# Kernel optimization log

Hardware: AMD Instinct MI355X
Metric: run time of the kernel (lower is better)

Reference implementation:

```python
import jax, jax.numpy as jnp
import numpy as np

# dims
B, N, M, R = 2, 16384, 512, 8      # batch, points, modes (slices), register tokens
D = 384                             # q_dim == kv_dim
H, DH = 8, 48                       # heads, dim_heads
P = 3                               # phys_dim
NF = DH // (2 * P)                  # rope freqs per physical axis (8)
FH = 1024                           # gated FFN hidden
L = 2                               # num_interleaved_layers
MINLF, MAXLF = -5.0, 3.0
EPS_LN = 1e-5
EPS_NORM = 1e-8


def _ln(x, g, b):
    m = jnp.mean(x, -1, keepdims=True)
    v = jnp.var(x, -1, keepdims=True)
    return (x - m) * jax.lax.rsqrt(v + EPS_LN) * g + b


def _rope_cs(coords):
    # coords: (B, S, P) -> cos/sin of shape (B, S, DH//2)
    freqs = jnp.exp(jnp.linspace(MINLF, MAXLF, NF))
    ang = (coords[..., :, None] * freqs).reshape(coords.shape[:-1] + (P * NF,))
    return jnp.cos(ang), jnp.sin(ang)


def _apply_rope(t, c, s):
    # t: (B, S, H, DH); c,s: (B, S, DH//2)
    tp = t.reshape(t.shape[:-1] + (DH // 2, 2))
    t0, t1 = tp[..., 0], tp[..., 1]
    c = c[:, :, None, :]
    s = s[:, :, None, :]
    r = jnp.stack([t0 * c - t1 * s, t0 * s + t1 * c], axis=-1)
    return r.reshape(t.shape)


def _mha(qin, kin, vin, xq, xk, wq, bq, wk, bk, wv, bv, wo, bo):
    Bq, Sq, _ = qin.shape
    Sk = kin.shape[1]
    q = (qin @ wq + bq).reshape(Bq, Sq, H, DH)
    k = (kin @ wk + bk).reshape(Bq, Sk, H, DH)
    v = (vin @ wv + bv).reshape(Bq, Sk, H, DH)
    cq, sq = _rope_cs(xq)
    ck, sk = _rope_cs(xk)
    q = _apply_rope(q, cq, sq)
    k = _apply_rope(k, ck, sk)
    scores = jnp.einsum('bqhd,bkhd->bhqk', q, k) / np.sqrt(DH).astype(np.float32)
    a = jax.nn.softmax(scores, axis=-1)
    o = jnp.einsum('bhqk,bkhd->bqhd', a, v).reshape(Bq, Sq, H * DH)
    return o @ wo + bo


def _subgen(feat, w, b):
    # Transolver slice generator: softmax over modes per point; mass == 1.
    tf = jax.nn.softmax(feat @ w + b, axis=-1)          # (B, S, M) trial_func
    tt = jnp.swapaxes(tf, 1, 2)                          # (B, M, S) trial_in_t
    inv = 1.0 / (jnp.sum(tf, axis=1) + EPS_NORM)         # (B, M) inv_trial_norm
    return tf, tt, inv[..., None]


def setup_inputs() -> dict:
    key = jax.random.key(0)
    ks = iter(jax.random.split(key, 64))
    nrm = lambda shape: jax.random.normal(next(ks), shape, dtype=jnp.float32)
    w = lambda shape: nrm(shape) * 0.02
    inp = {}
    inp['qx'] = nrm((B, N, D))
    inp['kvx'] = nrm((B, N, D))
    inp['x'] = jax.random.uniform(next(ks), (B, N, P), dtype=jnp.float32)
    inp['reg_tok_qx'] = nrm((B, R, D))
    inp['reg_tok_x'] = jax.random.uniform(next(ks), (B, R, P), dtype=jnp.float32)
    inp['subq_w'] = w((D, M)); inp['subq_b'] = jnp.zeros((M,))
    inp['subkv_w'] = w((D, M)); inp['subkv_b'] = jnp.zeros((M,))
    inp['nq_g'] = jnp.ones((D,)); inp['nq_b'] = jnp.zeros((D,))
    inp['nkv_g'] = jnp.ones((D,)); inp['nkv_b'] = jnp.zeros((D,))
    inp['a0_wq'] = w((D, H * DH)); inp['a0_bq'] = jnp.zeros((H * DH,))
    inp['a0_wk'] = w((D, H * DH)); inp['a0_bk'] = jnp.zeros((H * DH,))
    inp['a0_wv'] = w((D, H * DH)); inp['a0_bv'] = jnp.zeros((H * DH,))
    inp['a0_wo'] = w((H * DH, D)); inp['a0_bo'] = jnp.zeros((D,))
    inp['out_g'] = jnp.ones((D,)); inp['out_b'] = jnp.zeros((D,))
    inp['L_wq'] = w((L, D, H * DH)); inp['L_bq'] = jnp.zeros((L, H * DH))
    inp['L_wk'] = w((L, D, H * DH)); inp['L_bk'] = jnp.zeros((L, H * DH))
    inp['L_wv'] = w((L, D, H * DH)); inp['L_bv'] = jnp.zeros((L, H * DH))
    inp['L_wo'] = w((L, H * DH, D)); inp['L_bo'] = jnp.zeros((L, D))
    inp['L_ang'] = jnp.ones((L, D)); inp['L_anb'] = jnp.zeros((L, D))
    inp['L_fng'] = jnp.ones((L, D)); inp['L_fnb'] = jnp.zeros((L, D))
    inp['L_wg'] = w((L, D, FH)); inp['L_bg'] = jnp.zeros((L, FH))
    inp['L_wu'] = w((L, D, FH)); inp['L_bu'] = jnp.zeros((L, FH))
    inp['L_wd'] = w((L, FH, D)); inp['L_bd'] = jnp.zeros((L, D))
    return inp


def reference(qx, kvx, x, reg_tok_qx, reg_tok_x,
              subq_w, subq_b, subkv_w, subkv_b,
              nq_g, nq_b, nkv_g, nkv_b,
              a0_wq, a0_bq, a0_wk, a0_bk, a0_wv, a0_bv, a0_wo, a0_bo,
              out_g, out_b,
              L_wq, L_bq, L_wk, L_bk, L_wv, L_bv, L_wo, L_bo,
              L_ang, L_anb, L_fng, L_fnb,
              L_wg, L_bg, L_wu, L_bu, L_wd, L_bd):
    tfq, ttq, invq = _subgen(qx, subq_w, subq_b)
    _, ttkv, invkv = _subgen(kvx, subkv_w, subkv_b)
    qx_proj = jnp.matmul(ttq, qx) * invq          # (B, M, D)
    kvx_proj = jnp.matmul(ttkv, kvx) * invkv      # (B, M, D)
    xq_proj = jnp.matmul(ttq, x) * invq           # (B, M, P)
    xk_proj = jnp.matmul(ttkv, x) * invkv         # (B, M, P)
    q_full = jnp.concatenate([qx_proj, reg_tok_qx], axis=1)   # (B, M+R, D)
    xq_full = jnp.concatenate([xq_proj, reg_tok_x], axis=1)   # (B, M+R, P)
    q = _ln(q_full, nq_g, nq_b)
    kv = _ln(kvx_proj, nkv_g, nkv_b)
    y = _mha(q, kv, kv, xq_full, xk_proj,
             a0_wq, a0_bq, a0_wk, a0_bk, a0_wv, a0_bv, a0_wo, a0_bo) + q_full
    for i in range(L):
        h = _ln(y, L_fng[i], L_fnb[i])
        h = (jax.nn.silu(h @ L_wg[i] + L_bg[i]) * (h @ L_wu[i] + L_bu[i])) @ L_wd[i] + L_bd[i]
        y = h + y
        qn = _ln(y, L_ang[i], L_anb[i])
        y = _mha(qn, kv, kv, xq_full, xk_proj,
                 L_wq[i], L_bq[i], L_wk[i], L_bk[i], L_wv[i], L_bv[i], L_wo[i], L_bo[i]) + y
    y = _ln(y, out_g, out_b)
    y_proj = y[:, :M, :]
    reg_token = y[:, M:, :]
    y_recon = jnp.matmul(tfq, y_proj)             # (B, N, D)
    return (y_recon, reg_token)
```

## Files before the change

kernel.cpp:

```cpp
#include <hip/hip_runtime.h>


typedef __attribute__((ext_vector_type(8))) short short8;
typedef __attribute__((ext_vector_type(4))) float floatx4;

__device__ __forceinline__ float b2f(short s) {
    unsigned u = ((unsigned)(unsigned short)s) << 16;
    return __builtin_bit_cast(float, u);
}
__device__ __forceinline__ short f2b(float f) {
    unsigned u = __builtin_bit_cast(unsigned, f);
    unsigned r = (u + 0x7fffu + ((u >> 16) & 1u)) >> 16;
    return (short)r;
}

__device__ __forceinline__ void gload_lds16(const short* g, short* l) {
    __builtin_amdgcn_global_load_lds(
        (const __attribute__((address_space(1))) void*)(g),
        (__attribute__((address_space(3))) void*)(l), 16, 0, 0);
}

__global__ __launch_bounds__(256) void cvt_bf16(const float* __restrict__ src,
                                                short* __restrict__ dst, long n)
{
    long i = ((long)blockIdx.x * 256 + threadIdx.x) * 4;
    if (i + 4 <= n) {
        float4 v = *(const float4*)(src + i);
        short o[4] = {f2b(v.x), f2b(v.y), f2b(v.z), f2b(v.w)};
        *(short4*)(dst + i) = *(short4*)o;
    } else {
        for (long j = i; j < n; j++) dst[j] = f2b(src[j]);
    }
}

template <int EPI, bool SPLITK>
__global__ __launch_bounds__(256) void gemm_nt(
    const short* __restrict__ A, int lda, long sAb, long sAh,
    const short* __restrict__ Bm, int ldb, long sBb, long sBh,
    void* Cp, int ldc, long sCb, long sCh,
    const float* __restrict__ bias, int biasRow,
    const float* aux, int ldaux,
    int Mrows, int Ncols, int Kdim, int nb, int KC)
{
    int z = blockIdx.z;
    int b = z % nb;
    int rest = z / nb;
    long aoff = (long)b * sAb, boff = (long)b * sBb;
    long coff = (long)b * sCb + (long)rest * sCh;
    int k_begin = 0, kEnd = Kdim;
    if (SPLITK) {
        k_begin = rest * KC;
        int ke = k_begin + KC;
        kEnd = ke < Kdim ? ke : Kdim;
    } else {
        aoff += (long)rest * sAh;
        boff += (long)rest * sBh;
    }
    const short* Ap = A + aoff;
    const short* Bp = Bm + boff;

    int row0 = blockIdx.x * 128, col0 = blockIdx.y * 128;
    __shared__ __align__(16) short As[128 * 32];
    __shared__ __align__(16) short Bs[128 * 32];
    int tid = threadIdx.x, lane = tid & 63, wv = tid >> 6;
    int wr = (wv >> 1) * 64, wc = (wv & 1) * 64;
    int lr = lane & 15, lq = lane >> 4;

    const bool fullMN = (row0 + 128 <= Mrows) && (col0 + 128 <= Ncols);

    const int frow = (wv << 5) + (lane >> 2);
    const int fk = (lane & 3) << 3;
    const short* gA0 = Ap + (long)(row0 + frow) * lda + fk;
    const short* gA1 = gA0 + 16 * (long)lda;
    const short* gB0 = Bp + (long)(col0 + frow) * ldb + fk;
    const short* gB1 = gB0 + 16 * (long)ldb;
    short* lA0 = As + (wv << 10);
    short* lA1 = lA0 + 512;
    short* lB0 = Bs + (wv << 10);
    short* lB1 = lB0 + 512;

    floatx4 acc[4][4];
#pragma unroll
    for (int i = 0; i < 4; i++)
#pragma unroll
        for (int j = 0; j < 4; j++)
#pragma unroll
            for (int e = 0; e < 4; e++) acc[i][j][e] = 0.f;

    for (int k0 = k_begin; k0 < kEnd; k0 += 32) {
        __syncthreads();
        if (fullMN && (k0 + 32 <= kEnd)) {
            gload_lds16(gA0 + k0, lA0);
            gload_lds16(gA1 + k0, lA1);
            gload_lds16(gB0 + k0, lB0);
            gload_lds16(gB1 + k0, lB1);
        } else {
#pragma unroll
            for (int io = 0; io < 2; io++) {
                int sid = tid * 2 + io;
                int r = sid >> 2, sg = sid & 3;
                int gk = k0 + sg * 8;
                short8 va, vb;
#pragma unroll
                for (int j = 0; j < 8; j++) { va[j] = 0; vb[j] = 0; }
                int gra = row0 + r, grb = col0 + r;
                if (gra < Mrows) {
                    const short* p = Ap + (long)gra * lda + gk;
                    if (gk + 8 <= kEnd) va = *(const short8*)p;
                    else { for (int j = 0; j < 8; j++) if (gk + j < kEnd) va[j] = p[j]; }
                }
                if (grb < Ncols) {
                    const short* p = Bp + (long)grb * ldb + gk;
                    if (gk + 8 <= kEnd) vb = *(const short8*)p;
                    else { for (int j = 0; j < 8; j++) if (gk + j < kEnd) vb[j] = p[j]; }
                }
                *(short8*)&As[r * 32 + sg * 8] = va;
                *(short8*)&Bs[r * 32 + sg * 8] = vb;
            }
        }
        __syncthreads();
        short8 af[4], bfv[4];
#pragma unroll
        for (int mt = 0; mt < 4; mt++)
            af[mt] = *(const short8*)&As[(wr + mt * 16 + lr) * 32 + lq * 8];
#pragma unroll
        for (int nt = 0; nt < 4; nt++)
            bfv[nt] = *(const short8*)&Bs[(wc + nt * 16 + lr) * 32 + lq * 8];
#pragma unroll
        for (int mt = 0; mt < 4; mt++)
#pragma unroll
            for (int nt = 0; nt < 4; nt++)
                acc[mt][nt] = __builtin_amdgcn_mfma_f32_16x16x32_bf16(
                    af[mt], bfv[nt], acc[mt][nt], 0, 0, 0);
    }

    if (fullMN) {
#pragma unroll
        for (int mt = 0; mt < 4; mt++) {
#pragma unroll
            for (int nt = 0; nt < 4; nt++) {
                int gcol = col0 + wc + nt * 16 + lr;
#pragma unroll
                for (int r = 0; r < 4; r++) {
                    int grow = row0 + wr + mt * 16 + lq * 4 + r;
                    float v = acc[mt][nt][r];
                    if (bias) v += bias[biasRow ? grow : gcol];
                    long idx = coff + (long)grow * ldc + gcol;
                    if (EPI == 0) {
                        ((float*)Cp)[idx] = v;
                    } else if (EPI == 1) {
                        ((short*)Cp)[idx] = f2b(v);
                    } else if (EPI == 2) {
                        float g = aux[(long)grow * ldaux + gcol];
                        float sg = g / (1.f + __expf(-g));
                        ((short*)Cp)[idx] = f2b(sg * v);
                    } else {
                        float rr = aux[(long)grow * ldaux + gcol];
                        ((float*)Cp)[idx] = v + rr;
                    }
                }
            }
        }
    } else {
#pragma unroll
        for (int mt = 0; mt < 4; mt++) {
#pragma unroll
            for (int nt = 0; nt < 4; nt++) {
                int gcol = col0 + wc + nt * 16 + lr;
#pragma unroll
                for (int r = 0; r < 4; r++) {
                    int grow = row0 + wr + mt * 16 + lq * 4 + r;
                    if (grow < Mrows && gcol < Ncols) {
                        float v = acc[mt][nt][r];
                        if (bias) v += bias[biasRow ? grow : gcol];
                        long idx = coff + (long)grow * ldc + gcol;
                        if (EPI == 0) {
                            ((float*)Cp)[idx] = v;
                        } else if (EPI == 1) {
                            ((short*)Cp)[idx] = f2b(v);
                        } else if (EPI == 2) {
                            float g = aux[(long)grow * ldaux + gcol];
                            float sg = g / (1.f + __expf(-g));
                            ((short*)Cp)[idx] = f2b(sg * v);
                        } else {
                            float rr = aux[(long)grow * ldaux + gcol];
                            ((float*)Cp)[idx] = v + rr;
                        }
                    }
                }
            }
        }
    }
}

__global__ __launch_bounds__(256) void softmax_rows(
    const short* __restrict__ src, short* __restrict__ dstN,
    short* __restrict__ dstT, int rowsPerBatch)
{
    int n0 = blockIdx.x * 32;
    __shared__ __align__(16) short tile[32 * 512];
    int tid = threadIdx.x;
    const short8* gsrc = (const short8*)(src + (long)n0 * 512);
    short8* t8 = (short8*)tile;
#pragma unroll
    for (int i = 0; i < 8; i++) t8[tid + i * 256] = gsrc[tid + i * 256];
    __syncthreads();
    int wv = tid >> 6, lane = tid & 63;
#pragma unroll
    for (int rr = 0; rr < 8; rr++) {
        int r = wv * 8 + rr;
        short8 s = *(const short8*)&tile[r * 512 + lane * 8];
        float v[8];
        float mx = -1e30f;
#pragma unroll
        for (int j = 0; j < 8; j++) { v[j] = b2f(s[j]); mx = fmaxf(mx, v[j]); }
#pragma unroll
        for (int o = 32; o; o >>= 1) mx = fmaxf(mx, __shfl_xor(mx, o, 64));
        float sum = 0.f;
#pragma unroll
        for (int j = 0; j < 8; j++) { v[j] = __expf(v[j] - mx); sum += v[j]; }
#pragma unroll
        for (int o = 32; o; o >>= 1) sum += __shfl_xor(sum, o, 64);
        float inv = 1.0f / sum;
        short8 o8;
#pragma unroll
        for (int j = 0; j < 8; j++) o8[j] = f2b(v[j] * inv);
        *(short8*)&tile[r * 512 + lane * 8] = o8;
        if (dstN) *(short8*)(dstN + (long)(n0 + r) * 512 + lane * 8) = o8;
    }
    if (!dstT) return;
    __syncthreads();
    int b = n0 / rowsPerBatch;
    int nn0 = n0 % rowsPerBatch;
#pragma unroll
    for (int rep = 0; rep < 2; rep++) {
        int m = tid + rep * 256;
        short tmp[32];
#pragma unroll
        for (int i = 0; i < 32; i++) tmp[i] = tile[i * 512 + m];
        short* dst = dstT + ((long)b * 512 + m) * rowsPerBatch + nn0;
#pragma unroll
        for (int i = 0; i < 4; i++) *(short8*)(dst + i * 8) = *(const short8*)&tmp[i * 8];
    }
}

__global__ __launch_bounds__(256) void build_augT(
    const short* __restrict__ src, const float* __restrict__ xin,
    short* __restrict__ augT)
{
    int n0 = blockIdx.x * 32, jb = blockIdx.y, b = blockIdx.z;
    int t = threadIdx.x;
    if (jb == 12) {
        if (t < 128) {
            int jj = t >> 5, i = t & 31;
            float val = (jj < 3) ? xin[((long)b * 16384 + n0 + i) * 3 + jj] : 1.0f;
            augT[((long)(b * 512 + 384 + jj)) * 16384 + n0 + i] = f2b(val);
        }
        return;
    }
    __shared__ short tl[32][33];
    int j0 = jb * 32;
#pragma unroll
    for (int rep = 0; rep < 4; rep++) {
        int sid = t + rep * 256;
        int i = sid >> 5, j = sid & 31;
        tl[i][j] = src[((long)b * 16384 + n0 + i) * 384 + j0 + j];
    }
    __syncthreads();
#pragma unroll
    for (int rep = 0; rep < 4; rep++) {
        int sid = t + rep * 256;
        int j = sid >> 5, i = sid & 31;
        augT[((long)(b * 512 + j0 + j)) * 16384 + n0 + i] = tl[i][j];
    }
}

template <bool ISQ>
__global__ __launch_bounds__(256) void prep_kernel(
    const float* __restrict__ parts, const float* __restrict__ regqx,
    const float* __restrict__ regx, const float* __restrict__ gam,
    const float* __restrict__ bet, float* __restrict__ qfull,
    short* __restrict__ lnout, float* __restrict__ cb, float* __restrict__ sb,
    int Srows)
{
    int m = blockIdx.x, b = blockIdx.y, t = threadIdx.x;
    __shared__ float sh[388];
    __shared__ float r1[256], r2[256];
    bool isReg = ISQ && (m >= 512);
    if (isReg) {
        int rr = m - 512;
        for (int c = t; c < 384; c += 256) sh[c] = regqx[((long)b * 8 + rr) * 384 + c];
        if (t < 3) sh[384 + t] = regx[((long)b * 8 + rr) * 3 + t];
    } else {
        for (int c = t; c < 388; c += 256) {
            float s = 0.f;
#pragma unroll
            for (int sp = 0; sp < 8; sp++)
                s += parts[(((long)(sp * 2 + b)) * 512 + m) * 512 + c];
            sh[c] = s;
        }
    }
    __syncthreads();
    float inv = isReg ? 1.0f : 1.0f / (sh[387] + 1e-8f);
    float ls = 0.f, lq = 0.f;
    for (int c = t; c < 384; c += 256) {
        float v = sh[c] * inv;
        ls += v; lq += v * v;
    }
    r1[t] = ls; r2[t] = lq;
    __syncthreads();
    for (int o = 128; o; o >>= 1) {
        if (t < o) { r1[t] += r1[t + o]; r2[t] += r2[t + o]; }
        __syncthreads();
    }
    float mean = r1[0] * (1.f / 384.f);
    float var = r2[0] * (1.f / 384.f) - mean * mean;
    float rs = rsqrtf(var + 1e-5f);
    long row = (long)b * Srows + m;
    for (int c = t; c < 384; c += 256) {
        float v = sh[c] * inv;
        if (ISQ) qfull[row * 384 + c] = v;
        lnout[row * 384 + c] = f2b((v - mean) * rs * gam[c] + bet[c]);
    }
    if (t < 24) {
        int p = t >> 3, f = t & 7;
        float coord = sh[384 + p] * inv;
        float ang = coord * __expf(-5.0f + (float)f * (8.0f / 7.0f));
        cb[row * 24 + t] = cosf(ang);
        sb[row * 24 + t] = sinf(ang);
    }
}

struct TEntry { const float* src; short* dst; int rows, cols; };
struct TTable { TEntry e[20]; int cnt; };

__global__ __launch_bounds__(256) void transpose_many(TTable tab)
{
    int id = blockIdx.z;
    if (id >= tab.cnt) return;
    TEntry E = tab.e[id];
    int r0 = blockIdx.y * 32, c0 = blockIdx.x * 32;
    if (r0 >= E.rows || c0 >= E.cols) return;
    __shared__ short tl[32][33];
    int t = threadIdx.x;
#pragma unroll
    for (int rep = 0; rep < 4; rep++) {
        int sid = t + rep * 256;
        int i = sid >> 5, j = sid & 31;
        int r = r0 + i, c = c0 + j;
        tl[i][j] = (r < E.rows && c < E.cols) ? f2b(E.src[(long)r * E.cols + c])
                                              : (short)0;
    }
    __syncthreads();
#pragma unroll
    for (int rep = 0; rep < 4; rep++) {
        int sid = t + rep * 256;
        int j = sid >> 5, i = sid & 31;
        int c = c0 + j, r = r0 + i;
        if (c < E.cols && r < E.rows) E.dst[(long)c * E.rows + r] = tl[i][j];
    }
}

__global__ __launch_bounds__(256) void transpose_b16(
    const short* __restrict__ src, short* __restrict__ dst, int rows, int cols)
{
    int b = blockIdx.z;
    src += (long)b * rows * cols;
    dst += (long)b * rows * cols;
    int r0 = blockIdx.y * 32, c0 = blockIdx.x * 32;
    __shared__ short tl[32][33];
    int t = threadIdx.x;
#pragma unroll
    for (int rep = 0; rep < 4; rep++) {
        int sid = t + rep * 256;
        int i = sid >> 5, j = sid & 31;
        tl[i][j] = src[(long)(r0 + i) * cols + c0 + j];
    }
    __syncthreads();
#pragma unroll
    for (int rep = 0; rep < 4; rep++) {
        int sid = t + rep * 256;
        int j = sid >> 5, i = sid & 31;
        dst[(long)(c0 + j) * rows + r0 + i] = tl[i][j];
    }
}

__global__ __launch_bounds__(192) void rope_kernel(
    const float* __restrict__ pp, const float* __restrict__ cb,
    const float* __restrict__ sb, short* __restrict__ out, float scale)
{
    long row = blockIdx.x;
    int i = threadIdx.x;
    float c = cb[row * 24 + (i % 24)];
    float sn = sb[row * 24 + (i % 24)];
    float t0 = pp[row * 384 + 2 * i], t1 = pp[row * 384 + 2 * i + 1];
    out[row * 384 + 2 * i] = f2b((t0 * c - t1 * sn) * scale);
    out[row * 384 + 2 * i + 1] = f2b((t0 * sn + t1 * c) * scale);
}

__global__ __launch_bounds__(256) void attn_softmax(
    const float* __restrict__ Sc, short* __restrict__ P)
{
    int row = blockIdx.x * 4 + (threadIdx.x >> 6);
    int lane = threadIdx.x & 63;
    const float* sr = Sc + (long)row * 512 + lane * 8;
    float v[8];
    float mx = -1e30f;
#pragma unroll
    for (int j = 0; j < 8; j++) { v[j] = sr[j]; mx = fmaxf(mx, v[j]); }
#pragma unroll
    for (int o = 32; o; o >>= 1) mx = fmaxf(mx, __shfl_xor(mx, o, 64));
    float sum = 0.f;
#pragma unroll
    for (int j = 0; j < 8; j++) { v[j] = __expf(v[j] - mx); sum += v[j]; }
#pragma unroll
    for (int o = 32; o; o >>= 1) sum += __shfl_xor(sum, o, 64);
    float inv = 1.0f / sum;
    short8 o8;
#pragma unroll
    for (int j = 0; j < 8; j++) o8[j] = f2b(v[j] * inv);
    *(short8*)(P + (long)row * 512 + lane * 8) = o8;
}

__global__ __launch_bounds__(256) void ln_kernel(
    const float* __restrict__ in, const float* __restrict__ gam,
    const float* __restrict__ bet, short* __restrict__ out)
{
    long row = blockIdx.x;
    int t = threadIdx.x;
    const float* xr = in + row * 384;
    float v0 = xr[t];
    float v1 = (t < 128) ? xr[t + 256] : 0.f;
    __shared__ float r1[256], r2[256];
    r1[t] = v0 + v1; r2[t] = v0 * v0 + v1 * v1;
    __syncthreads();
    for (int o = 128; o; o >>= 1) {
        if (t < o) { r1[t] += r1[t + o]; r2[t] += r2[t + o]; }
        __syncthreads();
    }
    float mean = r1[0] * (1.f / 384.f);
    float var = r2[0] * (1.f / 384.f) - mean * mean;
    float rs = rsqrtf(var + 1e-5f);
    out[row * 384 + t] = f2b((v0 - mean) * rs * gam[t] + bet[t]);
    if (t < 128)
        out[row * 384 + t + 256] =
            f2b((v1 - mean) * rs * gam[t + 256] + bet[t + 256]);
}

__global__ __launch_bounds__(256) void outln_kernel(
    const float* __restrict__ in, const float* __restrict__ gam,
    const float* __restrict__ bet, short* __restrict__ yln,
    float* __restrict__ regout)
{
    int m = blockIdx.x, b = blockIdx.y, t = threadIdx.x;
    long row = (long)b * 520 + m;
    const float* xr = in + row * 384;
    float v0 = xr[t];
    float v1 = (t < 128) ? xr[t + 256] : 0.f;
    __shared__ float r1[256], r2[256];
    r1[t] = v0 + v1; r2[t] = v0 * v0 + v1 * v1;
    __syncthreads();
    for (int o = 128; o; o >>= 1) {
        if (t < o) { r1[t] += r1[t + o]; r2[t] += r2[t + o]; }
        __syncthreads();
    }
    float mean = r1[0] * (1.f / 384.f);
    float var = r2[0] * (1.f / 384.f) - mean * mean;
    float rs = rsqrtf(var + 1e-5f);
    float o0 = (v0 - mean) * rs * gam[t] + bet[t];
    if (m < 512) {
        yln[((long)b * 512 + m) * 384 + t] = f2b(o0);
        if (t < 128)
            yln[((long)b * 512 + m) * 384 + t + 256] =
                f2b((v1 - mean) * rs * gam[t + 256] + bet[t + 256]);
    } else {
        float* dst = regout + ((long)b * 8 + (m - 512)) * 384;
        dst[t] = o0;
        if (t < 128)
            dst[t + 256] = (v1 - mean) * rs * gam[t + 256] + bet[t + 256];
    }
}

__device__ __forceinline__ int chk3(float v, float lo, float hi) {
    if (!(v == v) || fabsf(v) > 3e38f) return 1;
    if (v < lo || v > hi) return 2;
    return 0;
}

__global__ __launch_bounds__(256) void probe_stages(
    const float* __restrict__ nqg, const float* __restrict__ qx,
    const short* __restrict__ subqT, const short* __restrict__ tfq,
    const float* __restrict__ qfull, const short* __restrict__ qln,
    const short* __restrict__ kvln, const float* __restrict__ cq,
    const short* __restrict__ Kr, const short* __restrict__ Pm,
    const short* __restrict__ Oc, const short* __restrict__ hg,
    const float* __restrict__ y, const short* __restrict__ ylnT,
    const float* __restrict__ dout, int* __restrict__ diag)
{
    int t = threadIdx.x;
    int task = blockIdx.x;
    __shared__ int sNaN, sRange, sPl;
    if (t == 0) { sNaN = 0; sRange = 0; sPl = 0; }
    __syncthreads();

    auto scanB = [&](const short* p, long n, float lo, float hi) {
        long stride = n / 2048; if (stride < 1) stride = 1;
        for (int j = 0; j < 8; j++) {
            long i = ((long)(t * 8 + j)) * stride;
            if (i >= n) break;
            int c = chk3(b2f(p[i]), lo, hi);
            if (c == 1) atomicOr(&sNaN, 1);
            else if (c == 2) atomicOr(&sRange, 1);
        }
    };
    auto scanF = [&](const float* p, long n, float lo, float hi) {
        long stride = n / 2048; if (stride < 1) stride = 1;
        for (int j = 0; j < 8; j++) {
            long i = ((long)(t * 8 + j)) * stride;
            if (i >= n) break;
            int c = chk3(p[i], lo, hi);
            if (c == 1) atomicOr(&sNaN, 1);
            else if (c == 2) atomicOr(&sRange, 1);
        }
    };

    int res = 0;
    if (task == 0) {
        int d1;
        {
            bool f32ones = true;
            for (int i = 0; i < 8; i++) if (nqg[i] != 1.0f) f32ones = false;
            d1 = f32ones ? 0 : 1;
        }
        int d2;
        {
            int plaus = 0;
            for (int i = 0; i < 64; i++) {
                float v = qx[i];
                float a = fabsf(v);
                if (v == v && a > 1e-4f && a < 16.f) plaus++;
            }
            d2 = (plaus >= 56) ? 0 : 1;
        }
        if (t == 0) diag[2] = d1 * 3 + d2;
        return;
    } else if (task == 1) {
        long n = 196608L;
        long stride = n / 2048; if (stride < 1) stride = 1;
        for (int j = 0; j < 8; j++) {
            long i = ((long)(t * 8 + j)) * stride;
            if (i >= n) break;
            float v = b2f(subqT[i]);
            float a = fabsf(v);
            if (!(v == v)) atomicOr(&sNaN, 1);
            else if (a >= 1e-7f && a <= 2.f) atomicAdd(&sPl, 1);
        }
        __syncthreads();
        res = sNaN ? 1 : ((sPl < 1228) ? 2 : 0);
        if (t == 0) diag[2 + 1] = res;
        return;
    }
    switch (task) {
        case 2: scanB(tfq, 16777216L, -1e-4f, 1.0001f); break;
        case 3: scanF(qfull, 399360L, -1e3f, 1e3f); break;
        case 4: scanB(qln, 399360L, -100.f, 100.f); break;
        case 5: scanB(kvln, 393216L, -100.f, 100.f); break;
        case 6: scanF(cq, 24960L, -1.0001f, 1.0001f); break;
        case 7: scanB(Kr, 399360L, -1e3f, 1e3f); break;
        case 8: scanB(Pm, 4259840L, -1e-4f, 1.0001f); break;
        case 9: scanB(Oc, 399360L, -1e3f, 1e3f); break;
        case 10: scanB(hg, 1064960L, -1e4f, 1e4f); break;
        case 11: scanF(y, 399360L, -1e5f, 1e5f); break;
        case 12: scanB(ylnT, 393216L, -100.f, 100.f); break;
        case 13: scanF(dout, 12589056L, -1e3f, 1e3f); break;
        default: break;
    }
    __syncthreads();
    res = sNaN ? 1 : (sRange ? 2 : 0);
    if (t == 0) diag[2 + task] = res;
}

__global__ void probe_combine(int* __restrict__ diag, unsigned wsMB)
{
    int firstBad = 0, kind = 0;
    for (int idx = 1; idx <= 13; idx++) {
        int r = diag[2 + idx];
        if (r != 0 && firstBad == 0) { firstBad = idx; kind = (r == 2) ? 1 : 0; }
    }
    int dd = diag[2];
    int wb;
    if (wsMB < 32) wb = 0; else if (wsMB < 48) wb = 1;
    else if (wsMB < 64) wb = 2; else if (wsMB < 80) wb = 3;
    else if (wsMB < 96) wb = 4; else if (wsMB < 100) wb = 5;
    else if (wsMB < 112) wb = 6; else if (wsMB < 128) wb = 7;
    else if (wsMB < 160) wb = 8; else if (wsMB < 224) wb = 9;
    else if (wsMB < 512) wb = 10; else wb = 11;

    int code = firstBad + 14 * (kind + 2 * (wb + 12 * dd));
    diag[0] = code;
    diag[1] = (firstBad == 0 && dd == 0) ? 1 : 0;
}

__global__ __launch_bounds__(256) void fill_out(float* __restrict__ out,
                                                const int* __restrict__ diag,
                                                long n)
{
    if (diag[1]) return;
    int code = diag[0];
    long i0 = ((long)blockIdx.x * 256 + threadIdx.x) * 8;
#pragma unroll
    for (int j = 0; j < 8; j++)
        if (i0 + j < n) out[i0 + j] = 0.f;
    if (i0 == 0)
        out[1] = ldexpf(1.0f + (float)(code & 255) * (1.0f / 256.0f),
                        (code >> 8) + 14);
}

#define LAUNCH_GEMM(EPI, SPLIT, GX, GY, GZ, A, LDA, SAB, SAH, B_, LDB, SBB,   \
                    SBH, C_, LDC, SCB, SCH, BIAS, BROW, AUX, LDAUX, M_, N_,   \
                    K_, NB, KC)                                               \
    gemm_nt<EPI, SPLIT><<<dim3(GX, GY, GZ), 256, 0, stream>>>(                \
        (const short*)(A), LDA, SAB, SAH, (const short*)(B_), LDB, SBB, SBH,  \
        (void*)(C_), LDC, SCB, SCH, (const float*)(BIAS), BROW,               \
        (const float*)(AUX), LDAUX, M_, N_, K_, NB, KC)

extern "C" void kernel_launch(void* const* d_in, const int* in_sizes, int n_in,
                              void* d_out, int out_size, void* d_ws,
                              size_t ws_size, hipStream_t stream)
{
    (void)in_sizes; (void)n_in; (void)out_size;
    const float* qx    = (const float*)d_in[0];
    const float* kvx   = (const float*)d_in[1];
    const float* xin   = (const float*)d_in[2];
    const float* regqx = (const float*)d_in[3];
    const float* regx  = (const float*)d_in[4];
    const float* subq_b  = (const float*)d_in[6];
    const float* subkv_b = (const float*)d_in[8];
    const float* nq_g = (const float*)d_in[9];
    const float* nq_b = (const float*)d_in[10];
    const float* nkv_g = (const float*)d_in[11];
    const float* nkv_b = (const float*)d_in[12];
    const float* a0_bq = (const float*)d_in[14];
    const float* a0_bk = (const float*)d_in[16];
    const float* a0_bv = (const float*)d_in[18];
    const float* a0_bo = (const float*)d_in[20];
    const float* out_g = (const float*)d_in[21];
    const float* out_b = (const float*)d_in[22];
    const float* L_bq = (const float*)d_in[24];
    const float* L_bk = (const float*)d_in[26];
    const float* L_bv = (const float*)d_in[28];
    const float* L_bo = (const float*)d_in[30];
    const float* L_ang = (const float*)d_in[31];
    const float* L_anb = (const float*)d_in[32];
    const float* L_fng = (const float*)d_in[33];
    const float* L_fnb = (const float*)d_in[34];
    const float* L_bg = (const float*)d_in[36];
    const float* L_bu = (const float*)d_in[38];
    const float* L_bd = (const float*)d_in[40];

    char* W = (char*)d_ws;
    short* qxb   = (short*)(W + 0L);
    short* kvxb  = (short*)(W + 25165824L);
    short* tfT   = (short*)(W + 50331648L);
    short* tfq   = (short*)(W + 83886080L);
    short* aug   = (short*)(W + 117440512L);
    float* parts = (float*)(W + 150994944L);
    short* Wt    = (short*)(W + 167772160L);
    float* qfull = (float*)(W + 176816128L);
    short* qln   = (short*)(W + 178413568L);
    short* kvln  = (short*)(W + 179212288L);
    float* cq    = (float*)(W + 179998720L);
    float* sq    = (float*)(W + 180098560L);
    float* ck    = (float*)(W + 180198400L);
    float* sk    = (float*)(W + 180296704L);
    float* y     = (float*)(W + 180395008L);
    short* hln   = (short*)(W + 181992448L);
    short* ylnT  = (short*)(W + 182791168L);
    float* Sc    = (float*)(W + 183577600L);
    short* Pm    = (short*)(W + 200616960L);
    float* gbuf  = (float*)(W + 209136640L);
    short* Oc    = (short*)(W + 213396480L);
    float* PP    = (float*)(W + 214195200L);
    short* Qr    = (short*)(W + 215792640L);
    short* Kr    = (short*)(W + 216591360L);
    short* Vt    = (short*)(W + 217377792L);
    short* hg    = (short*)(W + 218164224L);
    int*   diag  = (int*)(W + 220294144L);

    short* subqT  = Wt + 0L;
    short* subkvT = Wt + 196608L;
    short* a0qT   = Wt + 393216L;
    short* a0kT   = Wt + 540672L;
    short* a0vT   = Wt + 688128L;
    short* a0oT   = Wt + 835584L;
    auto WqT = [&](int l) { return Wt + 983040L + (long)l * 1769472L; };
    auto WkT = [&](int l) { return WqT(l) + 147456L; };
    auto WvT = [&](int l) { return WqT(l) + 294912L; };
    auto WoT = [&](int l) { return WqT(l) + 442368L; };
    auto WgT = [&](int l) { return WqT(l) + 589824L; };
    auto WuT = [&](int l) { return WqT(l) + 983040L; };
    auto WdT = [&](int l) { return WqT(l) + 1376256L; };

    cvt_bf16<<<12288, 256, 0, stream>>>(qx, qxb, 12582912L);
    cvt_bf16<<<12288, 256, 0, stream>>>(kvx, kvxb, 12582912L);

    TTable tt;
    int ti = 0;
    auto addT = [&](const void* s, short* dst, int r, int c) {
        tt.e[ti].src = (const float*)s; tt.e[ti].dst = dst;
        tt.e[ti].rows = r; tt.e[ti].cols = c; ti++;
    };
    addT(d_in[5], subqT, 384, 512);
    addT(d_in[7], subkvT, 384, 512);
    addT(d_in[13], a0qT, 384, 384);
    addT(d_in[15], a0kT, 384, 384);
    addT(d_in[17], a0vT, 384, 384);
    addT(d_in[19], a0oT, 384, 384);
    for (int l = 0; l < 2; l++) {
        addT((const float*)d_in[23] + (long)l * 147456, WqT(l), 384, 384);
        addT((const float*)d_in[25] + (long)l * 147456, WkT(l), 384, 384);
        addT((const float*)d_in[27] + (long)l * 147456, WvT(l), 384, 384);
        addT((const float*)d_in[29] + (long)l * 147456, WoT(l), 384, 384);
        addT((const float*)d_in[35] + (long)l * 393216, WgT(l), 384, 1024);
        addT((const float*)d_in[37] + (long)l * 393216, WuT(l), 384, 1024);
        addT((const float*)d_in[39] + (long)l * 393216, WdT(l), 1024, 384);
    }
    tt.cnt = ti;
    transpose_many<<<dim3(32, 32, 20), 256, 0, stream>>>(tt);

    LAUNCH_GEMM(1, false, 256, 4, 1, qxb, 384, 0L, 0L, subqT, 384, 0L, 0L,
                aug, 512, 0L, 0L, subq_b, 0, nullptr, 0, 32768, 512, 384, 1, 0);
    softmax_rows<<<1024, 256, 0, stream>>>(aug, tfq, tfT, 16384);
    build_augT<<<dim3(512, 13, 2), 256, 0, stream>>>(qxb, xin, aug);
    LAUNCH_GEMM(0, true, 4, 4, 16, tfT, 16384, 8388608L, 0L, aug, 16384,
                8388608L, 0L, parts, 512, 262144L, 524288L, nullptr, 0,
                nullptr, 0, 512, 388, 16384, 2, 2048);
    prep_kernel<true><<<dim3(520, 2), 256, 0, stream>>>(
        parts, regqx, regx, nq_g, nq_b, qfull, qln, cq, sq, 520);

    LAUNCH_GEMM(1, false, 256, 4, 1, kvxb, 384, 0L, 0L, subkvT, 384, 0L, 0L,
                aug, 512, 0L, 0L, subkv_b, 0, nullptr, 0, 32768, 512, 384, 1, 0);
    softmax_rows<<<1024, 256, 0, stream>>>(aug, nullptr, tfT, 16384);
    build_augT<<<dim3(512, 13, 2), 256, 0, stream>>>(kvxb, xin, aug);
    LAUNCH_GEMM(0, true, 4, 4, 16, tfT, 16384, 8388608L, 0L, aug, 16384,
                8388608L, 0L, parts, 512, 262144L, 524288L, nullptr, 0,
                nullptr, 0, 512, 388, 16384, 2, 2048);
    prep_kernel<false><<<dim3(512, 2), 256, 0, stream>>>(
        parts, nullptr, nullptr, nkv_g, nkv_b, nullptr, kvln, ck, sk, 512);

    const float qscale = 0.14433756729740643f;
    auto runMHA = [&](const short* qin, const short* wqT, const float* bq,
                      const short* wkT, const float* bk, const short* wvT,
                      const float* bv, const short* woT, const float* bo,
                      const float* res) {
        LAUNCH_GEMM(0, false, 9, 3, 1, qin, 384, 0L, 0L, wqT, 384, 0L, 0L, PP,
                    384, 0L, 0L, bq, 0, nullptr, 0, 1040, 384, 384, 1, 0);
        rope_kernel<<<1040, 192, 0, stream>>>(PP, cq, sq, Qr, qscale);
        LAUNCH_GEMM(0, false, 8, 3, 1, kvln, 384, 0L, 0L, wkT, 384, 0L, 0L, PP,
                    384, 0L, 0L, bk, 0, nullptr, 0, 1024, 384, 384, 1, 0);
        rope_kernel<<<1024, 192, 0, stream>>>(PP, ck, sk, Kr, 1.0f);
        LAUNCH_GEMM(1, false, 3, 4, 2, wvT, 384, 0L, 0L, kvln, 384, 196608L,
                    0L, Vt, 512, 196608L, 0L, bv, 1, nullptr, 0, 384, 512, 384,
                    2, 0);
        LAUNCH_GEMM(0, false, 5, 4, 16, Qr, 384, 199680L, 48L, Kr, 384,
                    196608L, 48L, Sc, 512, 2129920L, 266240L, nullptr, 0,
                    nullptr, 0, 520, 512, 48, 2, 0);
        attn_softmax<<<2080, 256, 0, stream>>>(Sc, Pm);
        LAUNCH_GEMM(1, false, 5, 1, 16, Pm, 512, 2129920L, 266240L, Vt, 512,
                    196608L, 24576L, Oc, 384, 199680L, 48L, nullptr, 0,
                    nullptr, 0, 520, 48, 512, 2, 0);
        LAUNCH_GEMM(3, false, 9, 3, 1, Oc, 384, 0L, 0L, woT, 384, 0L, 0L, y,
                    384, 0L, 0L, bo, 0, res, 384, 1040, 384, 384, 1, 0);
    };

    runMHA(qln, a0qT, a0_bq, a0kT, a0_bk, a0vT, a0_bv, a0oT, a0_bo, qfull);

    for (int l = 0; l < 2; l++) {
        ln_kernel<<<1040, 256, 0, stream>>>(y, L_fng + l * 384, L_fnb + l * 384, hln);
        LAUNCH_GEMM(0, false, 9, 8, 1, hln, 384, 0L, 0L, WgT(l), 384, 0L, 0L,
                    gbuf, 1024, 0L, 0L, L_bg + l * 1024, 0, nullptr, 0, 1040,
                    1024, 384, 1, 0);
        LAUNCH_GEMM(2, false, 9, 8, 1, hln, 384, 0L, 0L, WuT(l), 384, 0L, 0L,
                    hg, 1024, 0L, 0L, L_bu + l * 1024, 0, gbuf, 1024, 1040,
                    1024, 384, 1, 0);
        LAUNCH_GEMM(3, false, 9, 3, 1, hg, 1024, 0L, 0L, WdT(l), 1024, 0L, 0L,
                    y, 384, 0L, 0L, L_bd + l * 384, 0, y, 384, 1040, 384, 1024,
                    1, 0);
        ln_kernel<<<1040, 256, 0, stream>>>(y, L_ang + l * 384, L_anb + l * 384, hln);
        runMHA(hln, WqT(l), L_bq + l * 384, WkT(l), L_bk + l * 384, WvT(l),
               L_bv + l * 384, WoT(l), L_bo + l * 384, y);
    }

    short* yln = hln;
    float* regout = (float*)d_out + 12582912L;
    outln_kernel<<<dim3(520, 2), 256, 0, stream>>>(y, out_g, out_b, yln, regout);
    transpose_b16<<<dim3(12, 16, 2), 256, 0, stream>>>(yln, ylnT, 512, 384);
    LAUNCH_GEMM(0, false, 128, 3, 2, tfq, 512, 8388608L, 0L, ylnT, 512,
                196608L, 0L, (float*)d_out, 384, 6291456L, 0L, nullptr, 0,
                nullptr, 0, 16384, 384, 512, 2, 0);

    probe_stages<<<14, 256, 0, stream>>>(
        nq_g, qx, subqT, tfq, qfull, qln, kvln, cq, Kr, Pm, Oc, hg, y, ylnT,
        (const float*)d_out, diag);
    probe_combine<<<1, 1, 0, stream>>>(diag, (unsigned)(ws_size >> 20));
    fill_out<<<6147, 256, 0, stream>>>((float*)d_out, diag, 12589056L);
}
```

Measured before the change: 1.153 ms.

## Double-buffer GEMM LDS tiles and double split-K count for slice projections

The generic bf16 MFMA GEMM now uses two LDS buffers, issuing loads for the next K step before computing on the current one, with one barrier per iteration instead of two. The slice-projection GEMMs move from 16 to 32 K splits with chunk 1024, and N is padded to 512 so every tile takes the fast full-tile path. The parts buffer is relocated to fit 32 partials, and prep_kernel sums 16 partials per batch. This adds LDS usage (which may lower occupancy) and more partial-sum traffic in exchange for latency hiding and more parallelism.

```diff
diff --git a/kernel.cpp b/kernel.cpp
--- a/kernel.cpp
+++ b/kernel.cpp
@@ -60,8 +60,8 @@
     const short* Bp = Bm + boff;
 
     int row0 = blockIdx.x * 128, col0 = blockIdx.y * 128;
-    __shared__ __align__(16) short As[128 * 32];
-    __shared__ __align__(16) short Bs[128 * 32];
+    __shared__ __align__(16) short As[2 * 128 * 32];
+    __shared__ __align__(16) short Bs[2 * 128 * 32];
     int tid = threadIdx.x, lane = tid & 63, wv = tid >> 6;
     int wr = (wv >> 1) * 64, wc = (wv & 1) * 64;
     int lr = lane & 15, lq = lane >> 4;
@@ -79,22 +79,16 @@
     short* lB0 = Bs + (wv << 10);
     short* lB1 = lB0 + 512;
 
-    floatx4 acc[4][4];
-#pragma unroll
-    for (int i = 0; i < 4; i++)
-#pragma unroll
-        for (int j = 0; j < 4; j++)
-#pragma unroll
-            for (int e = 0; e < 4; e++) acc[i][j][e] = 0.f;
-
-    for (int k0 = k_begin; k0 < kEnd; k0 += 32) {
-        __syncthreads();
+    auto doStage = [&](int buf, int k0) {
         if (fullMN && (k0 + 32 <= kEnd)) {
-            gload_lds16(gA0 + k0, lA0);
-            gload_lds16(gA1 + k0, lA1);
-            gload_lds16(gB0 + k0, lB0);
-            gload_lds16(gB1 + k0, lB1);
+            int bo = buf << 12;
+            gload_lds16(gA0 + k0, lA0 + bo);
+            gload_lds16(gA1 + k0, lA1 + bo);
+            gload_lds16(gB0 + k0, lB0 + bo);
+            gload_lds16(gB1 + k0, lB1 + bo);
         } else {
+            short* Ab = As + (buf << 12);
+            short* Bb = Bs + (buf << 12);
 #pragma unroll
             for (int io = 0; io < 2; io++) {
                 int sid = tid * 2 + io;
@@ -114,24 +108,44 @@
                     if (gk + 8 <= kEnd) vb = *(const short8*)p;
                     else { for (int j = 0; j < 8; j++) if (gk + j < kEnd) vb[j] = p[j]; }
                 }
-                *(short8*)&As[r * 32 + sg * 8] = va;
-                *(short8*)&Bs[r * 32 + sg * 8] = vb;
+                *(short8*)&Ab[r * 32 + sg * 8] = va;
+                *(short8*)&Bb[r * 32 + sg * 8] = vb;
             }
         }
-        __syncthreads();
+    };
+
+    floatx4 acc[4][4];
+#pragma unroll
+    for (int i = 0; i < 4; i++)
+#pragma unroll
+        for (int j = 0; j < 4; j++)
+#pragma unroll
+            for (int e = 0; e < 4; e++) acc[i][j][e] = 0.f;
+
+    const int nSteps = (kEnd - k_begin + 31) >> 5;
+    doStage(0, k_begin);
+    __syncthreads();
+
+    for (int s = 0; s < nSteps; s++) {
+        const int cur = s & 1;
+        const int kn = k_begin + (s + 1) * 32;
+        if (s + 1 < nSteps) doStage(cur ^ 1, kn);
+
+        const int co = cur << 12;
         short8 af[4], bfv[4];
 #pragma unroll
         for (int mt = 0; mt < 4; mt++)
-            af[mt] = *(const short8*)&As[(wr + mt * 16 + lr) * 32 + lq * 8];
+            af[mt] = *(const short8*)&As[co + (wr + mt * 16 + lr) * 32 + lq * 8];
 #pragma unroll
         for (int nt = 0; nt < 4; nt++)
-            bfv[nt] = *(const short8*)&Bs[(wc + nt * 16 + lr) * 32 + lq * 8];
+            bfv[nt] = *(const short8*)&Bs[co + (wc + nt * 16 + lr) * 32 + lq * 8];
 #pragma unroll
         for (int mt = 0; mt < 4; mt++)
 #pragma unroll
             for (int nt = 0; nt < 4; nt++)
                 acc[mt][nt] = __builtin_amdgcn_mfma_f32_16x16x32_bf16(
                     af[mt], bfv[nt], acc[mt][nt], 0, 0, 0);
+        __syncthreads();
     }
 
     if (fullMN) {
@@ -295,7 +309,7 @@
         for (int c = t; c < 388; c += 256) {
             float s = 0.f;
 #pragma unroll
-            for (int sp = 0; sp < 8; sp++)
+            for (int sp = 0; sp < 16; sp++)
                 s += parts[(((long)(sp * 2 + b)) * 512 + m) * 512 + c];
             sh[c] = s;
         }
@@ -664,7 +678,6 @@
     short* tfT   = (short*)(W + 50331648L);
     short* tfq   = (short*)(W + 83886080L);
     short* aug   = (short*)(W + 117440512L);
-    float* parts = (float*)(W + 150994944L);
     short* Wt    = (short*)(W + 167772160L);
     float* qfull = (float*)(W + 176816128L);
     short* qln   = (short*)(W + 178413568L);
@@ -686,6 +699,7 @@
     short* Vt    = (short*)(W + 217377792L);
     short* hg    = (short*)(W + 218164224L);
     int*   diag  = (int*)(W + 220294144L);
+    float* parts = (float*)(W + 220298240L);
 
     short* subqT  = Wt + 0L;
     short* subkvT = Wt + 196608L;
@@ -732,9 +746,9 @@
                 aug, 512, 0L, 0L, subq_b, 0, nullptr, 0, 32768, 512, 384, 1, 0);
     softmax_rows<<<1024, 256, 0, stream>>>(aug, tfq, tfT, 16384);
     build_augT<<<dim3(512, 13, 2), 256, 0, stream>>>(qxb, xin, aug);
-    LAUNCH_GEMM(0, true, 4, 4, 16, tfT, 16384, 8388608L, 0L, aug, 16384,
+    LAUNCH_GEMM(0, true, 4, 4, 32, tfT, 16384, 8388608L, 0L, aug, 16384,
                 8388608L, 0L, parts, 512, 262144L, 524288L, nullptr, 0,
-                nullptr, 0, 512, 388, 16384, 2, 2048);
+                nullptr, 0, 512, 512, 16384, 2, 1024);
     prep_kernel<true><<<dim3(520, 2), 256, 0, stream>>>(
         parts, regqx, regx, nq_g, nq_b, qfull, qln, cq, sq, 520);
 
@@ -742,9 +756,9 @@
                 aug, 512, 0L, 0L, subkv_b, 0, nullptr, 0, 32768, 512, 384, 1, 0);
     softmax_rows<<<1024, 256, 0, stream>>>(aug, nullptr, tfT, 16384);
     build_augT<<<dim3(512, 13, 2), 256, 0, stream>>>(kvxb, xin, aug);
-    LAUNCH_GEMM(0, true, 4, 4, 16, tfT, 16384, 8388608L, 0L, aug, 16384,
+    LAUNCH_GEMM(0, true, 4, 4, 32, tfT, 16384, 8388608L, 0L, aug, 16384,
                 8388608L, 0L, parts, 512, 262144L, 524288L, nullptr, 0,
-                nullptr, 0, 512, 388, 16384, 2, 2048);
+                nullptr, 0, 512, 512, 16384, 2, 1024);
     prep_kernel<false><<<dim3(512, 2), 256, 0, stream>>>(
         parts, nullptr, nullptr, nkv_g, nkv_b, nullptr, kvln, ck, sk, 512);
 
```

New measurement: 1.122 ms. 1.03x faster.
